# Kernel optimization log

Measured on AMD Instinct MI355X. Metric: run time of the kernel, lower is better.

The kernel has to match this reference:

```python
import jax, jax.numpy as jnp
import numpy as np

N_NODES = 100000
N_EDGES = 1600000
IN_DIM = 165
HIDDEN = 128
OUT_DIM = 2


def gcn_conv(x, W, b, src, dst, n_nodes):
    """PyG GCNConv: h = x @ W; add self-loops; sym-normalized scatter-add; + bias."""
    h = x @ W  # [N, F_out]
    loop = jnp.arange(n_nodes, dtype=src.dtype)
    src_f = jnp.concatenate([src, loop])  # [E + N]
    dst_f = jnp.concatenate([dst, loop])
    deg = jax.ops.segment_sum(jnp.ones(src_f.shape[0], dtype=h.dtype), dst_f,
                              num_segments=n_nodes)  # in-degree incl. self-loop
    dinv = jnp.where(deg > 0, jax.lax.rsqrt(deg), jnp.zeros_like(deg))
    norm = dinv[src_f] * dinv[dst_f]  # [E + N]
    msg = h[src_f] * norm[:, None]  # gather + scale, [E+N, F_out]
    out = jax.ops.segment_sum(msg, dst_f, num_segments=n_nodes)  # scatter-add
    return out + b


def setup_inputs() -> dict:
    key = jax.random.key(0)
    k_x, k_e, k_w1, k_b1, k_w2, k_b2 = jax.random.split(key, 6)
    x = jax.random.normal(k_x, (N_NODES, IN_DIM), dtype=jnp.float32)
    edge_index = jax.random.randint(k_e, (2, N_EDGES), 0, N_NODES, dtype=jnp.int64)
    # Glorot-like init for linear weights, zeros for bias (PyG defaults)
    W1 = jax.random.normal(k_w1, (IN_DIM, HIDDEN), dtype=jnp.float32) / np.sqrt(IN_DIM)
    b1 = jnp.zeros((HIDDEN,), dtype=jnp.float32)
    W2 = jax.random.normal(k_w2, (HIDDEN, OUT_DIM), dtype=jnp.float32) / np.sqrt(HIDDEN)
    b2 = jnp.zeros((OUT_DIM,), dtype=jnp.float32)
    return {"x": x, "edge_index": edge_index, "W1": W1, "b1": b1, "W2": W2, "b2": b2}


def reference(x, edge_index, W1, b1, W2, b2):
    src, dst = edge_index[0], edge_index[1]
    h = gcn_conv(x, W1, b1, src, dst, N_NODES)
    h = jax.nn.relu(h)
    # dropout: eval mode (training=False) -> identity
    out = gcn_conv(h, W2, b2, src, dst, N_NODES)
    return out
```

## Files before the change

### kernel.cpp

```cpp
#include <hip/hip_runtime.h>
#include <hip/hip_fp16.h>

#define N_NODES 100000
#define N_EDGES 1600000
#define IN_DIM  165
#define HIDDEN  128
#define OUT_DIM 2

#define NBKT 196
#define CHUNK 8192
#define NCHUNK ((N_EDGES + CHUNK - 1) / CHUNK)
#define PADCAP 10240
#define KPAD 176

typedef _Float16 half8_t __attribute__((ext_vector_type(8)));
typedef _Float16 half4_t __attribute__((ext_vector_type(4)));
typedef float floatx4 __attribute__((ext_vector_type(4)));


__global__ __launch_bounds__(256) void k_part2(const int* __restrict__ src,
                                               const int* __restrict__ dst,
                                               int* __restrict__ bcnt,
                                               unsigned* __restrict__ arena) {
    __shared__ unsigned stage[CHUNK];
    __shared__ int hist[256];
    __shared__ int startv[256];
    __shared__ int lcur[256];
    __shared__ int gbase[256];
    __shared__ int wsum[4];

    int t = threadIdx.x;
    int lane = t & 63, wid = t >> 6;
    int e0 = blockIdx.x * CHUNK;
    int nE = N_EDGES - e0; if (nE > CHUNK) nE = CHUNK;

    hist[t] = 0;
    __syncthreads();

    for (int i = t; i < nE; i += 256)
        atomicAdd(&hist[dst[e0 + i] >> 9], 1);
    __syncthreads();

    int v = hist[t];
    int inc = v;
    #pragma unroll
    for (int off = 1; off < 64; off <<= 1) {
        int y = __shfl_up(inc, off);
        if (lane >= off) inc += y;
    }
    if (lane == 63) wsum[wid] = inc;
    __syncthreads();
    if (t == 0) {
        int acc = 0;
        #pragma unroll
        for (int w = 0; w < 4; w++) { int tv = wsum[w]; wsum[w] = acc; acc += tv; }
    }
    __syncthreads();
    int excl = wsum[wid] + inc - v;
    startv[t] = excl;
    lcur[t] = excl;
    if (t < NBKT && v > 0) gbase[t] = t * PADCAP + atomicAdd(&bcnt[t], v);
    __syncthreads();

    for (int i = t; i < nE; i += 256) {
        int d = dst[e0 + i];
        int s = src[e0 + i];
        int bk = d >> 9;
        unsigned entry = (unsigned)s | ((unsigned)(d & 511) << 17);
        int pos = atomicAdd(&lcur[bk], 1);
        stage[pos] = entry;
    }
    __syncthreads();

    for (int bk = wid; bk < NBKT; bk += 4) {
        int cnt = hist[bk];
        int lo = startv[bk];
        int gb = gbase[bk];
        for (int j = lane; j < cnt; j += 64)
            arena[gb + j] = stage[lo + j];
    }
}


__global__ __launch_bounds__(256) void k_btot(const int* __restrict__ bcnt,
                                              int* __restrict__ bucketptr) {
    __shared__ int wsum[4];
    int t = threadIdx.x, lane = t & 63, wid = t >> 6;
    int v = (t < NBKT) ? bcnt[t] : 0;
    int inc = v;
    #pragma unroll
    for (int off = 1; off < 64; off <<= 1) {
        int y = __shfl_up(inc, off);
        if (lane >= off) inc += y;
    }
    if (lane == 63) wsum[wid] = inc;
    __syncthreads();
    if (t == 0) {
        int acc = 0;
        #pragma unroll
        for (int w = 0; w < 4; w++) { int tv = wsum[w]; wsum[w] = acc; acc += tv; }
    }
    __syncthreads();
    int excl = wsum[wid] + inc - v;
    if (t <= NBKT) bucketptr[t] = (t < NBKT) ? excl : N_EDGES;
}


__global__ __launch_bounds__(256) void k_sort3(const unsigned* __restrict__ arena,
                                               const int* __restrict__ bcnt,
                                               const int* __restrict__ bucketptr,
                                               int* __restrict__ csr,
                                               int* __restrict__ rowptr,
                                               float* __restrict__ dinv) {
    __shared__ int cnt[512];
    __shared__ int cur[512];
    __shared__ int wsum[4];
    int b = blockIdx.x;
    int n0 = b << 9;
    int t = threadIdx.x;
    int lane = t & 63, wid = t >> 6;
    int total = bcnt[b];
    int abase = b * PADCAP;
    int dbase = bucketptr[b];

    cnt[t] = 0;
    cnt[t + 256] = 0;
    __syncthreads();
    for (int p = t; p < total; p += 256)
        atomicAdd(&cnt[arena[abase + p] >> 17], 1);
    __syncthreads();

    int c0 = cnt[2 * t], c1 = cnt[2 * t + 1];
    int s = c0 + c1;
    int inc = s;
    #pragma unroll
    for (int off = 1; off < 64; off <<= 1) {
        int y = __shfl_up(inc, off);
        if (lane >= off) inc += y;
    }
    if (lane == 63) wsum[wid] = inc;
    __syncthreads();
    if (t == 0) {
        int acc = 0;
        #pragma unroll
        for (int w = 0; w < 4; w++) { int tv = wsum[w]; wsum[w] = acc; acc += tv; }
    }
    __syncthreads();
    int base = dbase + wsum[wid] + (inc - s);
    cur[2 * t] = base;
    cur[2 * t + 1] = base + c0;
    int node0 = n0 + 2 * t;
    if (node0 < N_NODES) {
        rowptr[node0] = base;
        dinv[node0] = rsqrtf((float)(c0 + 1));
    }
    if (node0 + 1 < N_NODES) {
        rowptr[node0 + 1] = base + c0;
        dinv[node0 + 1] = rsqrtf((float)(c1 + 1));
    }
    if (b == NBKT - 1 && t == 0) rowptr[N_NODES] = N_EDGES;
    __syncthreads();

    for (int p = t; p < total; p += 256) {
        unsigned entry = arena[abase + p];
        int local = (int)(entry >> 17);
        int sv = (int)(entry & 0x1FFFFu);
        int pos = atomicAdd(&cur[local], 1);
        csr[pos] = sv;
    }
}


__global__ void k_w1t(const float* __restrict__ W1, _Float16* __restrict__ w1t) {
    int idx = blockIdx.x * 256 + threadIdx.x;
    if (idx < HIDDEN * KPAD) {
        int c = idx / KPAD, k = idx - c * KPAD;
        float v = (k < IN_DIM) ? W1[k * HIDDEN + c] : 0.f;
        w1t[idx] = (_Float16)v;
    }
}


__global__ __launch_bounds__(256) void k_gemm1(const float* __restrict__ x,
                                               const _Float16* __restrict__ w1t,
                                               const float* __restrict__ dinv,
                                               _Float16* __restrict__ h1s) {
    int t = threadIdx.x;
    int wid = t >> 6, lane = t & 63;
    int row0 = (blockIdx.x * 4 + wid) * 16;
    if (row0 >= N_NODES) return;
    int m = lane & 15;
    int quad = lane >> 4;
    const float* xrow = x + (size_t)(row0 + m) * IN_DIM;

    floatx4 acc[8];
    #pragma unroll
    for (int i = 0; i < 8; i++) acc[i] = (floatx4)(0.f);

    #pragma unroll
    for (int kc = 0; kc < 5; kc++) {
        int kb = kc * 32 + quad * 8;
        half8_t a;
        #pragma unroll
        for (int j = 0; j < 8; j++) a[j] = (_Float16)xrow[kb + j];
        #pragma unroll
        for (int cb = 0; cb < 8; cb++) {
            int col = cb * 16 + m;
            half8_t bf = *(const half8_t*)&w1t[col * KPAD + kb];
            acc[cb] = __builtin_amdgcn_mfma_f32_16x16x32_f16(a, bf, acc[cb], 0, 0, 0);
        }
    }
    {
        int kb = 160 + quad * 4;
        half4_t a;
        #pragma unroll
        for (int j = 0; j < 4; j++)
            a[j] = (kb + j < IN_DIM) ? (_Float16)xrow[kb + j] : (_Float16)0.f;
        #pragma unroll
        for (int cb = 0; cb < 8; cb++) {
            int col = cb * 16 + m;
            half4_t bf = *(const half4_t*)&w1t[col * KPAD + kb];
            acc[cb] = __builtin_amdgcn_mfma_f32_16x16x16f16(a, bf, acc[cb], 0, 0, 0);
        }
    }
    float dv[4];
    #pragma unroll
    for (int r = 0; r < 4; r++) dv[r] = dinv[row0 + quad * 4 + r];
    #pragma unroll
    for (int cb = 0; cb < 8; cb++) {
        #pragma unroll
        for (int r = 0; r < 4; r++) {
            h1s[(size_t)(row0 + quad * 4 + r) * HIDDEN + cb * 16 + m] =
                (_Float16)(acc[cb][r] * dv[r]);
        }
    }
}


__global__ __launch_bounds__(256) void k_agg1(const __half2* __restrict__ h1,
                                              const int* __restrict__ rowptr,
                                              const int* __restrict__ csr,
                                              const float* __restrict__ dinv,
                                              const float* __restrict__ b1,
                                              const float* __restrict__ W2,
                                              float2* __restrict__ h2s) {
    int node = blockIdx.x * 4 + (threadIdx.x >> 6);
    int f = threadIdx.x & 63;
    float2 self = __half22float2(h1[node * 64 + f]);
    float accx = self.x, accy = self.y;
    int p0 = rowptr[node], p1 = rowptr[node + 1];

    int p = p0;
    for (; p + 7 < p1; p += 8) {
        int s[8];
        #pragma unroll
        for (int j = 0; j < 8; j++) s[j] = csr[p + j];
        __half2 g[8];
        #pragma unroll
        for (int j = 0; j < 8; j++) g[j] = h1[s[j] * 64 + f];
        #pragma unroll
        for (int j = 0; j < 8; j++) {
            float2 gf = __half22float2(g[j]);
            accx += gf.x;
            accy += gf.y;
        }
    }
    for (; p < p1; p++) {
        float2 gf = __half22float2(h1[csr[p] * 64 + f]);
        accx += gf.x;
        accy += gf.y;
    }

    float di = dinv[node];
    float2 bb = ((const float2*)b1)[f];
    float z0 = fmaf(di, accx, bb.x);
    float z1 = fmaf(di, accy, bb.y);
    float r0 = fmaxf(z0, 0.f);
    float r1 = fmaxf(z1, 0.f);
    float4 w2v = ((const float4*)W2)[f];
    float a0 = r0 * w2v.x + r1 * w2v.z;
    float a1 = r0 * w2v.y + r1 * w2v.w;
    #pragma unroll
    for (int off = 32; off; off >>= 1) {
        a0 += __shfl_down(a0, off);
        a1 += __shfl_down(a1, off);
    }
    if (f == 0) h2s[node] = make_float2(di * a0, di * a1);
}


__global__ void k_agg2(const float2* __restrict__ h2s, const int* __restrict__ rowptr,
                       const int* __restrict__ csr, const float* __restrict__ dinv,
                       const float* __restrict__ b2, float2* __restrict__ out) {
    int i = blockIdx.x * blockDim.x + threadIdx.x;
    if (i >= N_NODES) return;
    float2 self = h2s[i];
    float a0 = self.x, a1 = self.y;
    int p0 = rowptr[i], p1 = rowptr[i + 1];
    int p = p0;
    for (; p + 3 < p1; p += 4) {
        int s0 = csr[p], s1 = csr[p + 1], s2 = csr[p + 2], s3 = csr[p + 3];
        float2 g0 = h2s[s0], g1 = h2s[s1], g2 = h2s[s2], g3 = h2s[s3];
        a0 += g0.x + g1.x + g2.x + g3.x;
        a1 += g0.y + g1.y + g2.y + g3.y;
    }
    for (; p < p1; p++) {
        float2 g = h2s[csr[p]];
        a0 += g.x;
        a1 += g.y;
    }
    float di = dinv[i];
    out[i] = make_float2(fmaf(di, a0, b2[0]), fmaf(di, a1, b2[1]));
}


extern "C" void kernel_launch(void* const* d_in, const int* in_sizes, int n_in,
                              void* d_out, int out_size, void* d_ws, size_t ws_size,
                              hipStream_t stream) {
    const float* x  = (const float*)d_in[0];
    const int*   ei = (const int*)d_in[1];
    const float* W1 = (const float*)d_in[2];
    const float* b1 = (const float*)d_in[3];
    const float* W2 = (const float*)d_in[4];
    const float* b2 = (const float*)d_in[5];
    float* out = (float*)d_out;

    const int* src = ei;
    const int* dst = ei + N_EDGES;

    char* ws = (char*)d_ws;
    size_t off = 0;
    auto alloc = [&](size_t bytes) -> void* {
        void* p = ws + off;
        off += (bytes + 255) & ~(size_t)255;
        return p;
    };
    _Float16* h1s    = (_Float16*)alloc((size_t)N_NODES * HIDDEN * 2);
    float*    dinv   = (float*)   alloc((size_t)N_NODES * 4);
    int*      rowptr = (int*)     alloc((size_t)(N_NODES + 1) * 4);
    int*      bcnt   = (int*)     alloc((size_t)NBKT * 4);
    int*      bktptr = (int*)     alloc((size_t)(NBKT + 1) * 4);
    unsigned* arena  = (unsigned*)alloc((size_t)NBKT * PADCAP * 4);
    int*      csr    = (int*)     alloc((size_t)N_EDGES * 4);
    _Float16* w1t    = (_Float16*)alloc((size_t)HIDDEN * KPAD * 2);
    float2*   h2s    = (float2*)  alloc((size_t)N_NODES * 8);

    (void)hipMemsetAsync(bcnt, 0, (size_t)NBKT * 4, stream);
    k_w1t<<<(HIDDEN * KPAD + 255) / 256, 256, 0, stream>>>(W1, w1t);
    k_part2<<<NCHUNK, 256, 0, stream>>>(src, dst, bcnt, arena);
    k_btot<<<1, 256, 0, stream>>>(bcnt, bktptr);
    k_sort3<<<NBKT, 256, 0, stream>>>(arena, bcnt, bktptr, csr, rowptr, dinv);
    k_gemm1<<<(N_NODES / 16 + 3) / 4, 256, 0, stream>>>(x, w1t, dinv, h1s);
    k_agg1<<<N_NODES / 4, 256, 0, stream>>>((const __half2*)h1s, rowptr, csr, dinv, b1, W2, h2s);
    k_agg2<<<(N_NODES + 255) / 256, 256, 0, stream>>>(h2s, rowptr, csr, dinv, b2, (float2*)out);
}
```

Before: 285.7 us.

## Scatter partition entries directly to global arena and widen sort blocks

The partition kernel drops its shared-memory staging buffer and local prefix scan; each edge instead takes a per-bucket slot via a shared atomic and writes straight into the global arena, with half-size chunks and 512 threads per block. The sort kernel moves to 1024 threads per block, with only the first 256 threads doing the scan. This removes an LDS staging pass and two barriers, but the arena writes become scattered instead of coalesced per bucket, and ordering within buckets becomes nondeterministic.

```diff
diff --git a/kernel.cpp b/kernel.cpp
--- a/kernel.cpp
+++ b/kernel.cpp
@@ -8,7 +8,7 @@
 #define OUT_DIM 2
 
 #define NBKT 196
-#define CHUNK 8192
+#define CHUNK 4096
 #define NCHUNK ((N_EDGES + CHUNK - 1) / CHUNK)
 #define PADCAP 10240
 #define KPAD 176
@@ -18,66 +18,35 @@
 typedef float floatx4 __attribute__((ext_vector_type(4)));
 
 
-__global__ __launch_bounds__(256) void k_part2(const int* __restrict__ src,
+__global__ __launch_bounds__(512) void k_part2(const int* __restrict__ src,
                                                const int* __restrict__ dst,
                                                int* __restrict__ bcnt,
                                                unsigned* __restrict__ arena) {
-    __shared__ unsigned stage[CHUNK];
     __shared__ int hist[256];
-    __shared__ int startv[256];
-    __shared__ int lcur[256];
     __shared__ int gbase[256];
-    __shared__ int wsum[4];
 
     int t = threadIdx.x;
-    int lane = t & 63, wid = t >> 6;
     int e0 = blockIdx.x * CHUNK;
     int nE = N_EDGES - e0; if (nE > CHUNK) nE = CHUNK;
 
-    hist[t] = 0;
-    __syncthreads();
-
-    for (int i = t; i < nE; i += 256)
+    if (t < 256) hist[t] = 0;
+    __syncthreads();
+
+    for (int i = t; i < nE; i += 512)
         atomicAdd(&hist[dst[e0 + i] >> 9], 1);
     __syncthreads();
 
-    int v = hist[t];
-    int inc = v;
-    #pragma unroll
-    for (int off = 1; off < 64; off <<= 1) {
-        int y = __shfl_up(inc, off);
-        if (lane >= off) inc += y;
-    }
-    if (lane == 63) wsum[wid] = inc;
-    __syncthreads();
-    if (t == 0) {
-        int acc = 0;
-        #pragma unroll
-        for (int w = 0; w < 4; w++) { int tv = wsum[w]; wsum[w] = acc; acc += tv; }
-    }
-    __syncthreads();
-    int excl = wsum[wid] + inc - v;
-    startv[t] = excl;
-    lcur[t] = excl;
-    if (t < NBKT && v > 0) gbase[t] = t * PADCAP + atomicAdd(&bcnt[t], v);
-    __syncthreads();
-
-    for (int i = t; i < nE; i += 256) {
+    if (t < NBKT) gbase[t] = t * PADCAP + atomicAdd(&bcnt[t], hist[t]);
+    if (t < 256) hist[t] = 0;
+    __syncthreads();
+
+    for (int i = t; i < nE; i += 512) {
         int d = dst[e0 + i];
         int s = src[e0 + i];
         int bk = d >> 9;
         unsigned entry = (unsigned)s | ((unsigned)(d & 511) << 17);
-        int pos = atomicAdd(&lcur[bk], 1);
-        stage[pos] = entry;
-    }
-    __syncthreads();
-
-    for (int bk = wid; bk < NBKT; bk += 4) {
-        int cnt = hist[bk];
-        int lo = startv[bk];
-        int gb = gbase[bk];
-        for (int j = lane; j < cnt; j += 64)
-            arena[gb + j] = stage[lo + j];
+        int idx = atomicAdd(&hist[bk], 1);
+        arena[gbase[bk] + idx] = entry;
     }
 }
 
@@ -106,12 +75,12 @@
 }
 
 
-__global__ __launch_bounds__(256) void k_sort3(const unsigned* __restrict__ arena,
-                                               const int* __restrict__ bcnt,
-                                               const int* __restrict__ bucketptr,
-                                               int* __restrict__ csr,
-                                               int* __restrict__ rowptr,
-                                               float* __restrict__ dinv) {
+__global__ __launch_bounds__(1024) void k_sort3(const unsigned* __restrict__ arena,
+                                                const int* __restrict__ bcnt,
+                                                const int* __restrict__ bucketptr,
+                                                int* __restrict__ csr,
+                                                int* __restrict__ rowptr,
+                                                float* __restrict__ dinv) {
     __shared__ int cnt[512];
     __shared__ int cur[512];
     __shared__ int wsum[4];
@@ -123,22 +92,25 @@
     int abase = b * PADCAP;
     int dbase = bucketptr[b];
 
-    cnt[t] = 0;
-    cnt[t + 256] = 0;
-    __syncthreads();
-    for (int p = t; p < total; p += 256)
+    if (t < 512) cnt[t] = 0;
+    __syncthreads();
+    for (int p = t; p < total; p += 1024)
         atomicAdd(&cnt[arena[abase + p] >> 17], 1);
     __syncthreads();
 
-    int c0 = cnt[2 * t], c1 = cnt[2 * t + 1];
-    int s = c0 + c1;
-    int inc = s;
-    #pragma unroll
-    for (int off = 1; off < 64; off <<= 1) {
-        int y = __shfl_up(inc, off);
-        if (lane >= off) inc += y;
-    }
-    if (lane == 63) wsum[wid] = inc;
+    int c0 = 0, c1 = 0, s = 0, inc = 0;
+    if (t < 256) {
+        c0 = cnt[2 * t];
+        c1 = cnt[2 * t + 1];
+        s = c0 + c1;
+        inc = s;
+        #pragma unroll
+        for (int off = 1; off < 64; off <<= 1) {
+            int y = __shfl_up(inc, off);
+            if (lane >= off) inc += y;
+        }
+        if (lane == 63) wsum[wid] = inc;
+    }
     __syncthreads();
     if (t == 0) {
         int acc = 0;
@@ -146,22 +118,24 @@
         for (int w = 0; w < 4; w++) { int tv = wsum[w]; wsum[w] = acc; acc += tv; }
     }
     __syncthreads();
-    int base = dbase + wsum[wid] + (inc - s);
-    cur[2 * t] = base;
-    cur[2 * t + 1] = base + c0;
-    int node0 = n0 + 2 * t;
-    if (node0 < N_NODES) {
-        rowptr[node0] = base;
-        dinv[node0] = rsqrtf((float)(c0 + 1));
-    }
-    if (node0 + 1 < N_NODES) {
-        rowptr[node0 + 1] = base + c0;
-        dinv[node0 + 1] = rsqrtf((float)(c1 + 1));
+    if (t < 256) {
+        int base = dbase + wsum[wid] + (inc - s);
+        cur[2 * t] = base;
+        cur[2 * t + 1] = base + c0;
+        int node0 = n0 + 2 * t;
+        if (node0 < N_NODES) {
+            rowptr[node0] = base;
+            dinv[node0] = rsqrtf((float)(c0 + 1));
+        }
+        if (node0 + 1 < N_NODES) {
+            rowptr[node0 + 1] = base + c0;
+            dinv[node0 + 1] = rsqrtf((float)(c1 + 1));
+        }
     }
     if (b == NBKT - 1 && t == 0) rowptr[N_NODES] = N_EDGES;
     __syncthreads();
 
-    for (int p = t; p < total; p += 256) {
+    for (int p = t; p < total; p += 1024) {
         unsigned entry = arena[abase + p];
         int local = (int)(entry >> 17);
         int sv = (int)(entry & 0x1FFFFu);
@@ -347,9 +321,9 @@
 
     (void)hipMemsetAsync(bcnt, 0, (size_t)NBKT * 4, stream);
     k_w1t<<<(HIDDEN * KPAD + 255) / 256, 256, 0, stream>>>(W1, w1t);
-    k_part2<<<NCHUNK, 256, 0, stream>>>(src, dst, bcnt, arena);
+    k_part2<<<NCHUNK, 512, 0, stream>>>(src, dst, bcnt, arena);
     k_btot<<<1, 256, 0, stream>>>(bcnt, bktptr);
-    k_sort3<<<NBKT, 256, 0, stream>>>(arena, bcnt, bktptr, csr, rowptr, dinv);
+    k_sort3<<<NBKT, 1024, 0, stream>>>(arena, bcnt, bktptr, csr, rowptr, dinv);
     k_gemm1<<<(N_NODES / 16 + 3) / 4, 256, 0, stream>>>(x, w1t, dinv, h1s);
     k_agg1<<<N_NODES / 4, 256, 0, stream>>>((const __half2*)h1s, rowptr, csr, dinv, b1, W2, h2s);
     k_agg2<<<(N_NODES + 255) / 256, 256, 0, stream>>>(h2s, rowptr, csr, dinv, b2, (float2*)out);
```

Result: faster. 266.2 us (-6.8%).
